# Kernel tuning notes

Measured on AMD Instinct MI355X. Metric: run time of the kernel, lower is better.

Reference implementation:

```python
import jax, jax.numpy as jnp
import numpy as np

B, S, D_IN, D_OUT = 4, 4096, 1024, 1024

def setup_inputs() -> dict:
    key = jax.random.key(0)
    kx, kq, kk, kv = jax.random.split(key, 4)
    x = jax.random.normal(kx, (B, S, D_IN), dtype=jnp.float32)
    # torch nn.Linear stores weight as [d_out, d_in]; y = x @ W.T
    Wq = jax.random.normal(kq, (D_OUT, D_IN), dtype=jnp.float32) * 0.02
    Wk = jax.random.normal(kk, (D_OUT, D_IN), dtype=jnp.float32) * 0.02
    Wv = jax.random.normal(kv, (D_OUT, D_IN), dtype=jnp.float32) * 0.02
    return {"x": x, "Wq": Wq, "Wk": Wk, "Wv": Wv}

def reference(x, Wq, Wk, Wv):
    b, n, _ = x.shape
    d_out = Wk.shape[0]
    q = jnp.einsum('bnd,od->bno', x, Wq)
    k = jnp.einsum('bnd,od->bno', x, Wk)
    v = jnp.einsum('bnd,od->bno', x, Wv)
    scores = jnp.einsum('bqo,bko->bqk', q, k)  # [B, S, S]
    causal = jnp.triu(jnp.ones((n, n), dtype=bool), k=1)
    scores = jnp.where(causal, -jnp.inf, scores)
    attn = jax.nn.softmax(scores / jnp.sqrt(jnp.float32(d_out)), axis=-1)
    # dropout p=0.0 -> identity
    return jnp.einsum('bqk,bko->bqo', attn, v)
```

## Files before the change

### kernel.cpp

```cpp
#include <hip/hip_runtime.h>


typedef unsigned short u16;
typedef unsigned int u32;
typedef __attribute__((ext_vector_type(8))) short bf16x8;
typedef __attribute__((ext_vector_type(4))) float f32x4;
typedef __attribute__((ext_vector_type(8))) unsigned short u16x8;

__device__ __forceinline__ u16 f2bf(float f) {
  union { float f; unsigned u; } v; v.f = f;
  unsigned r = v.u + 0x7FFFu + ((v.u >> 16) & 1u);
  return (u16)(r >> 16);
}
__device__ __forceinline__ float bf2f(u16 h) {
  union { unsigned u; float f; } v; v.u = ((unsigned)h) << 16;
  return v.f;
}
__device__ __forceinline__ f32x4 mfma16(bf16x8 a, bf16x8 b, f32x4 c) {
  return __builtin_amdgcn_mfma_f32_16x16x32_bf16(a, b, c, 0, 0, 0);
}
__device__ __forceinline__ void gld_lds16(const u16* g, u16* l) {
  __builtin_amdgcn_global_load_lds(
      (const __attribute__((address_space(1))) u32*)g,
      (__attribute__((address_space(3))) u32*)l, 16, 0, 0);
}
#define BAR() do { __builtin_amdgcn_s_barrier(); \
                   __builtin_amdgcn_sched_barrier(0); } while (0)
#define LGKM0() do { asm volatile("s_waitcnt lgkmcnt(0)" ::: "memory"); \
                     __builtin_amdgcn_sched_barrier(0); } while (0)
#define VMC(n) asm volatile("s_waitcnt vmcnt(" #n ")" ::: "memory")

__global__ __launch_bounds__(256)
void cast_all(const float* __restrict__ x, const float* __restrict__ Wq,
              const float* __restrict__ Wk, const float* __restrict__ Wv,
              u16* __restrict__ wX, u16* __restrict__ wWqkv) {
  int i = blockIdx.x * 256 + threadIdx.x;
  const float* src; u16* dst; int j;
  if (i < 2097152)        { src = x;  dst = wX;                j = i; }
  else if (i < 2228224)   { src = Wq; dst = wWqkv;             j = i - 2097152; }
  else if (i < 2359296)   { src = Wk; dst = wWqkv + 1048576;   j = i - 2228224; }
  else if (i < 2490368)   { src = Wv; dst = wWqkv + 2097152;   j = i - 2359296; }
  else return;
  const float4* s4 = (const float4*)src;
  float4 a = s4[2*j], b = s4[2*j+1];
  u16x8 o;
  o[0]=f2bf(a.x); o[1]=f2bf(a.y); o[2]=f2bf(a.z); o[3]=f2bf(a.w);
  o[4]=f2bf(b.x); o[5]=f2bf(b.y); o[6]=f2bf(b.z); o[7]=f2bf(b.w);
  ((u16x8*)dst)[j] = o;
}

#define GEMM8_CORE(Abase, Bbase)                                              \
  auto stageA = [&](int bufi, int h, int t) {                                 \
    _Pragma("unroll")                                                         \
    for (int i = 0; i < 2; ++i) {                                             \
      int ci = i * 512 + tid;                                                 \
      int r  = ci >> 3;                                                       \
      int c  = (ci & 7) ^ (r & 7);                                            \
      gld_lds16(Abase + (size_t)(h * 128 + r) * 1024 + t * 64 + c * 8,        \
                &At[bufi][h][ci * 8]);                                        \
    }                                                                         \
  };                                                                          \
  auto stageB = [&](int bufi, int h, int t) {                                 \
    _Pragma("unroll")                                                         \
    for (int i = 0; i < 2; ++i) {                                             \
      int ci = i * 512 + tid;                                                 \
      int r  = ci >> 3;                                                       \
      int c  = (ci & 7) ^ (r & 7);                                            \
      gld_lds16(Bbase + (size_t)(h * 128 + r) * 1024 + t * 64 + c * 8,        \
                &Bt[bufi][h][ci * 8]);                                        \
    }                                                                         \
  };                                                                          \
  bf16x8 af[8][2], bfr[4][2];                                                 \
  auto readA = [&](int bufi, int mb) {                                        \
    _Pragma("unroll")                                                         \
    for (int m = 0; m < 4; ++m)                                               \
      _Pragma("unroll")                                                       \
      for (int dk = 0; dk < 2; ++dk) {                                        \
        int r  = (mb + m) * 16 + c16;                                         \
        int ch = dk * 4 + g;                                                  \
        af[mb + m][dk] =                                                      \
            *(const bf16x8*)&At[bufi][wr][r * 64 + ((ch ^ (r & 7)) * 8)];     \
      }                                                                       \
  };                                                                          \
  auto readB = [&](int bufi, int nb) {                                        \
    _Pragma("unroll")                                                         \
    for (int n = 0; n < 2; ++n)                                               \
      _Pragma("unroll")                                                       \
      for (int dk = 0; dk < 2; ++dk) {                                        \
        int r  = (wc & 1) * 64 + (nb + n) * 16 + c16;                         \
        int ch = dk * 4 + g;                                                  \
        bfr[nb + n][dk] =                                                     \
            *(const bf16x8*)&Bt[bufi][wc >> 1][r * 64 + ((ch ^ (r & 7)) * 8)];\
      }                                                                       \
  };                                                                          \
  auto domfma = [&](int mb, int nb) {                                         \
    __builtin_amdgcn_s_setprio(1);                                            \
    _Pragma("unroll")                                                         \
    for (int dk = 0; dk < 2; ++dk)                                            \
      _Pragma("unroll")                                                       \
      for (int m = 0; m < 4; ++m)                                             \
        _Pragma("unroll")                                                     \
        for (int n = 0; n < 2; ++n)                                           \
          acc[mb + m][nb + n] =                                               \
              mfma16(af[mb + m][dk], bfr[nb + n][dk], acc[mb + m][nb + n]);   \
    __builtin_amdgcn_s_setprio(0);                                            \
  };                                                                          \
                   \
  stageA(0, 0, 0); stageA(0, 1, 0); stageB(0, 0, 0); stageB(0, 1, 0);         \
  stageA(1, 0, 1); stageA(1, 1, 1); stageB(1, 0, 1); stageB(1, 1, 1);         \
  VMC(8);                                         \
  BAR();                                                                      \
  for (int it = 0; it < 8; ++it) {                                            \
    const bool pf = (it < 7);                                                 \
    const int t2 = 2 * it + 2, t3 = 2 * it + 3;                               \
                                   \
    readA(0, 0); readB(0, 0);                                                 \
    BAR(); LGKM0();                                                           \
    domfma(0, 0);                                                             \
    BAR();                                                                    \
                                   \
    readA(0, 4);                                                              \
    BAR(); LGKM0();                                                           \
    domfma(4, 0);                                                             \
    BAR();                                                                    \
                     \
    readB(0, 2);                                                              \
    if (pf) { stageA(0, 0, t2); stageA(0, 1, t2); }                           \
    BAR(); LGKM0();                                                           \
    domfma(4, 2);                                                             \
    BAR();                                                                    \
                         \
    if (pf) { stageB(0, 0, t2); stageB(0, 1, t2); }                           \
    BAR();                                                                    \
    domfma(0, 2);                                                             \
    if (pf) { VMC(8); } else { VMC(0); }                                      \
    BAR();                                                                    \
                                                   \
    readA(1, 0); readB(1, 0);                                                 \
    BAR(); LGKM0();                                                           \
    domfma(0, 0);                                                             \
    BAR();                                                                    \
    readA(1, 4);                                                              \
    BAR(); LGKM0();                                                           \
    domfma(4, 0);                                                             \
    BAR();                                                                    \
    readB(1, 2);                                                              \
    if (pf) { stageA(1, 0, t3); stageA(1, 1, t3); }                           \
    BAR(); LGKM0();                                                           \
    domfma(4, 2);                                                             \
    BAR();                                                                    \
    if (pf) { stageB(1, 0, t3); stageB(1, 1, t3); }                           \
    BAR();                                                                    \
    domfma(0, 2);                                                             \
    if (pf) { VMC(8); } else { VMC(0); }                                      \
    BAR();                                                                    \
  }

__global__ __launch_bounds__(512, 1)
void qkv_gemm(const u16* __restrict__ X, const u16* __restrict__ W,
              u16* __restrict__ Qo, u16* __restrict__ Ko, u16* __restrict__ VTo) {
  __shared__ __align__(16) u16 At[2][2][128 * 64];
  __shared__ __align__(16) u16 Bt[2][2][128 * 64];
  const int tid = threadIdx.x;
  const int w = tid >> 6, lane = tid & 63;
  const int g = lane >> 4, c16 = lane & 15;
  const int wr = w >> 2, wc = w & 3;
  const int lid = blockIdx.x;
  const int xcd = lid & 7, gg = lid >> 3;
  const int M0 = ((xcd << 3) | (gg & 7)) * 256;
  const int N0 = (gg >> 3) * 256;
  const u16* Abase = X + (size_t)M0 * 1024;
  const u16* Bbase = W + (size_t)N0 * 1024;

  f32x4 acc[8][4] = {};
  GEMM8_CORE(Abase, Bbase);

  const int which = N0 >> 10;
  const int colbase = N0 & 1023;
#pragma unroll
  for (int m = 0; m < 8; ++m) {
#pragma unroll
    for (int n = 0; n < 4; ++n) {
#pragma unroll
      for (int r = 0; r < 4; ++r) {
        int gm  = M0 + wr * 128 + m * 16 + 4 * g + r;
        int col = colbase + wc * 64 + n * 16 + c16;
        u16 hv = f2bf(acc[m][n][r]);
        if (which == 0) {
          Qo[(size_t)gm * 1024 + col] = hv;
        } else if (which == 1) {
          Ko[(size_t)gm * 1024 + col] = hv;
        } else {
          int b = gm >> 12, s2 = gm & 4095;
          VTo[((size_t)((b << 10) + col)) * 4096 + s2] = hv;
        }
      }
    }
  }
}

__global__ __launch_bounds__(512, 1)
void sgemm_exp(const u16* __restrict__ Q, const u16* __restrict__ K,
               u16* __restrict__ Spack, float* __restrict__ lpart) {
  __shared__ __align__(16) u16 At[2][2][128 * 64];
  __shared__ __align__(16) u16 Bt[2][2][128 * 64];
  __shared__ float lsum[256][4];
  const int tid = threadIdx.x;
  const int w = tid >> 6, lane = tid & 63;
  const int g = lane >> 4, c16 = lane & 15;
  const int wr = w >> 2, wc = w & 3;
  const int b = blockIdx.y;

  int L = (blockIdx.x & 7) * 17 + (blockIdx.x >> 3);
  int qt = 0;
  while ((qt + 1) * (qt + 2) / 2 <= L) ++qt;
  const int kt = L - qt * (qt + 1) / 2;

  const u16* Abase = Q + (size_t)b * 4096 * 1024 + (size_t)qt * 256 * 1024;
  const u16* Bbase = K + (size_t)b * 4096 * 1024 + (size_t)kt * 256 * 1024;

  f32x4 acc[8][4] = {};
  GEMM8_CORE(Abase, Bbase);

  const int qt128 = 2 * qt + wr;
  const int kt128 = 2 * kt + (wc >> 1);
  const bool exists = (kt128 <= qt128);
  u16* Sb = Spack + (((size_t)b * 528 + (size_t)(qt128 * (qt128 + 1)) / 2 + kt128) << 14);
  const int q0 = qt * 256, k0g = kt * 256;
  float psum[8][4];
#pragma unroll
  for (int m = 0; m < 8; ++m)
#pragma unroll
    for (int r = 0; r < 4; ++r) psum[m][r] = 0.f;
#pragma unroll
  for (int m = 0; m < 8; ++m) {
#pragma unroll
    for (int n = 0; n < 4; ++n) {
#pragma unroll
      for (int r = 0; r < 4; ++r) {
        int rl = wr * 128 + m * 16 + 4 * g + r;
        int cl = wc * 64 + n * 16 + c16;
        float s = acc[m][n][r] * 0.03125f;
        float p = (k0g + cl <= q0 + rl) ? __expf(s) : 0.f;
        u16 pb = f2bf(p);
        if (exists) Sb[(rl & 127) * 128 + (cl & 127)] = pb;
        psum[m][r] += bf2f(pb);
      }
    }
  }
#pragma unroll
  for (int m = 0; m < 8; ++m)
#pragma unroll
    for (int r = 0; r < 4; ++r) {
      float v = psum[m][r];
      v += __shfl_xor(v, 1, 64);
      v += __shfl_xor(v, 2, 64);
      v += __shfl_xor(v, 4, 64);
      v += __shfl_xor(v, 8, 64);
      psum[m][r] = v;
    }
  if (c16 == 0) {
#pragma unroll
    for (int m = 0; m < 8; ++m)
#pragma unroll
      for (int r = 0; r < 4; ++r)
        lsum[wr * 128 + m * 16 + 4 * g + r][wc] = psum[m][r];
  }
  __syncthreads();
  if (tid < 256) {
    float v = lsum[tid][0] + lsum[tid][1] + lsum[tid][2] + lsum[tid][3];
    lpart[((size_t)b * 4096 + q0 + tid) * 16 + kt] = v;
  }
}

__global__ __launch_bounds__(512)
void pv_gemm(const u16* __restrict__ Spack, const u16* __restrict__ VT,
             const u16* __restrict__ ztile, const float* __restrict__ lpart,
             float* __restrict__ Out) {
  __shared__ __align__(16) u16 At[2][256 * 64];
  __shared__ __align__(16) u16 Bt[2][128 * 64];
  __shared__ float linv_lds[512];
  const int tid = threadIdx.x;
  const int w = tid >> 6, lane = tid & 63;
  const int g = lane >> 4, c16 = lane & 15;
  const int wm = w >> 1, wn = w & 1;
  const int pp = blockIdx.x;
  const int d0 = blockIdx.y;
  const int b  = blockIdx.z;

  const u16* Sp_b = Spack + (size_t)b * 528 * 16384;
  const u16* VTb  = VT + (size_t)b * 1024 * 4096;
  float* Ob = Out + (size_t)b * 4096 * 1024;

  {
    const int QTr = (tid < 256) ? pp : (15 - pp);
    const int row = QTr * 256 + (tid & 255);
    const int nt  = QTr + 1;
    const float* p = lpart + ((size_t)b * 4096 + row) * 16;
    float s = 0.f;
    for (int i = 0; i < nt; ++i) s += p[i];
    linv_lds[tid] = 1.f / s;
  }

  for (int pass = 0; pass < 2; ++pass) {
    const int QT = pass == 0 ? pp : 15 - pp;
    const int M0 = QT * 256;
    const int nsteps = (QT + 1) * 4;
    const int tLo = 2 * QT;
    const size_t triLo = (size_t)(tLo * (tLo + 1)) / 2;
    const size_t triHi = (size_t)((tLo + 1) * (tLo + 2)) / 2;

    f32x4 acc[4][4] = {};

    auto stage = [&](int s, int tt) {
      const int kv0 = tt * 64;
      const int kt128 = tt >> 1;
      const int koff = (tt & 1) * 64;
      const u16* baseLo = (kt128 <= tLo) ? Sp_b + ((triLo + kt128) << 14) : ztile;
      const u16* baseHi = Sp_b + ((triHi + kt128) << 14);
#pragma unroll
      for (int i = 0; i < 4; ++i) {
        int ci = i * 512 + tid;
        int r = ci >> 3;
        int c = (ci & 7) ^ (r & 7);
        const u16* base = (i < 2) ? baseLo : baseHi;
        gld_lds16(base + (size_t)(r & 127) * 128 + koff + c * 8, &At[s][ci * 8]);
      }
#pragma unroll
      for (int i = 0; i < 2; ++i) {
        int ci = i * 512 + tid;
        int r = ci >> 3;
        int c = (ci & 7) ^ (r & 7);
        gld_lds16(VTb + (size_t)(d0 * 128 + r) * 4096 + kv0 + c * 8, &Bt[s][ci * 8]);
      }
    };
    auto compute = [&](int s) {
#pragma unroll
      for (int dk = 0; dk < 2; ++dk) {
        bf16x8 af2[4], bf2[4];
#pragma unroll
        for (int m = 0; m < 4; ++m) {
          int row = wm * 64 + m * 16 + c16;
          int ch = dk * 4 + g;
          af2[m] = *(const bf16x8*)&At[s][row * 64 + ((ch ^ (row & 7)) * 8)];
        }
#pragma unroll
        for (int n = 0; n < 4; ++n) {
          int row = wn * 64 + n * 16 + c16;
          int ch = dk * 4 + g;
          bf2[n] = *(const bf16x8*)&Bt[s][row * 64 + ((ch ^ (row & 7)) * 8)];
        }
#pragma unroll
        for (int m = 0; m < 4; ++m)
#pragma unroll
          for (int n = 0; n < 4; ++n)
            acc[m][n] = mfma16(af2[m], bf2[n], acc[m][n]);
      }
    };

    stage(0, 0);
    __syncthreads();
    int cur = 0;
    for (int t = 0; t < nsteps; ++t) {
      if (t + 1 < nsteps) stage(cur ^ 1, t + 1);
      compute(cur);
      __syncthreads();
      cur ^= 1;
    }

    const float* lb = linv_lds + pass * 256;
#pragma unroll
    for (int m = 0; m < 4; ++m) {
#pragma unroll
      for (int r = 0; r < 4; ++r) {
        int rl = wm * 64 + m * 16 + 4 * g + r;
        float li = lb[rl];
#pragma unroll
        for (int n = 0; n < 4; ++n) {
          int dcol = d0 * 128 + wn * 64 + n * 16 + c16;
          Ob[(size_t)(M0 + rl) * 1024 + dcol] = acc[m][n][r] * li;
        }
      }
    }
  }
}

__global__ __launch_bounds__(512, 2)
void attn_kernel(const u16* __restrict__ Q, const u16* __restrict__ K,
                 const u16* __restrict__ VT, float* __restrict__ Out) {
  __shared__ u16 kv_lds[32 * 1024];
  __shared__ float s_part[4][32][33];
  __shared__ u16 p_lds[32 * 40];
  __shared__ float l_lds[32];

  const int tid = threadIdx.x;
  const int w = tid >> 6, lane = tid & 63;
  const int g = lane >> 4, c16 = lane & 15;
  const int b  = blockIdx.x & 3;
  const int qb = 127 - (blockIdx.x >> 2);
  const int qs = qb * 32;
  const int kh = w & 1, dq = w >> 1;

  const u16* Qb  = Q  + (size_t)b * 4096 * 1024;
  const u16* Kb  = K  + (size_t)b * 4096 * 1024;
  const u16* VTb = VT + (size_t)b * 1024 * 4096;

  bf16x8 qfrag[2][8];
#pragma unroll
  for (int qh = 0; qh < 2; ++qh)
#pragma unroll
    for (int dk = 0; dk < 8; ++dk)
      qfrag[qh][dk] = *(const bf16x8*)(Qb + (size_t)(qs + qh * 16 + c16) * 1024
                                       + dq * 256 + dk * 32 + g * 8);

  f32x4 oacc[2][8] = {};
  if (tid < 32) l_lds[tid] = 0.f;

  const int qrow_p = tid >> 4;
  const int kk     = tid & 15;
  const int gq     = qs + qrow_p;

  for (int j = 0; j <= qb; ++j) {
    const int kv0 = j * 32;
    __syncthreads();
    uint4 rk[8];
#pragma unroll
    for (int i = 0; i < 8; ++i) {
      int ci = i * 512 + tid;
      int r  = ci >> 7;
      int c  = (ci & 127) ^ (r & 7);
      rk[i] = *(const uint4*)(Kb + (size_t)(kv0 + r) * 1024 + c * 8);
    }
#pragma unroll
    for (int i = 0; i < 8; ++i)
      *(uint4*)&kv_lds[(size_t)(i * 512 + tid) * 8] = rk[i];
    __syncthreads();
    f32x4 sacc[2] = {};
#pragma unroll
    for (int dk = 0; dk < 8; ++dk) {
      int kvrow = kh * 16 + c16;
      int ch    = dq * 32 + dk * 4 + g;
      bf16x8 kf = *(const bf16x8*)&kv_lds[kvrow * 1024 + ((ch ^ (kvrow & 7)) * 8)];
      sacc[0] = mfma16(qfrag[0][dk], kf, sacc[0]);
      sacc[1] = mfma16(qfrag[1][dk], kf, sacc[1]);
    }
#pragma unroll
    for (int qh = 0; qh < 2; ++qh)
#pragma unroll
      for (int r = 0; r < 4; ++r)
        s_part[dq][qh * 16 + 4 * g + r][kh * 16 + c16] = sacc[qh][r];
    __syncthreads();
    uint4 rv[8];
#pragma unroll
    for (int i = 0; i < 8; ++i) {
      int ci = i * 512 + tid;
      int d  = ((ci >> 6) << 4) + (ci & 15);
      int c  = (ci >> 4) & 3;
      rv[i] = *(const uint4*)(VTb + (size_t)d * 4096 + kv0 + c * 8);
    }
    {
      float psum = 0.f;
#pragma unroll
      for (int h = 0; h < 2; ++h) {
        int kcol = kk + h * 16;
        float s = s_part[0][qrow_p][kcol] + s_part[1][qrow_p][kcol]
                + s_part[2][qrow_p][kcol] + s_part[3][qrow_p][kcol];
        s *= 0.03125f;
        float p = (kv0 + kcol <= gq) ? __expf(s) : 0.f;
        u16 pb = f2bf(p);
        p_lds[qrow_p * 40 + kcol] = pb;
        psum += bf2f(pb);
      }
#pragma unroll
      for (int off = 1; off < 16; off <<= 1)
        psum += __shfl_xor(psum, off, 64);
      if (kk == 0) l_lds[qrow_p] += psum;
    }
#pragma unroll
    for (int i = 0; i < 8; ++i)
      *(uint4*)&kv_lds[(size_t)(i * 512 + tid) * 8] = rv[i];
    __syncthreads();
    bf16x8 pa0 = *(const bf16x8*)&p_lds[(0  + c16) * 40 + g * 8];
    bf16x8 pa1 = *(const bf16x8*)&p_lds[(16 + c16) * 40 + g * 8];
#pragma unroll
    for (int f = 0; f < 8; ++f) {
      int dcol = w * 128 + f * 16 + c16;
      int pos  = (dcol >> 4) * 64 + g * 16 + (dcol & 15);
      bf16x8 vf = *(const bf16x8*)&kv_lds[(size_t)pos * 8];
      oacc[0][f] = mfma16(pa0, vf, oacc[0][f]);
      oacc[1][f] = mfma16(pa1, vf, oacc[1][f]);
    }
  }

  float* Ob = Out + (size_t)b * 4096 * 1024;
#pragma unroll
  for (int qh = 0; qh < 2; ++qh) {
#pragma unroll
    for (int r = 0; r < 4; ++r) {
      int ql = qh * 16 + 4 * g + r;
      float linvv = 1.f / l_lds[ql];
#pragma unroll
      for (int f = 0; f < 8; ++f)
        Ob[(size_t)(qs + ql) * 1024 + w * 128 + f * 16 + c16] = oacc[qh][f][r] * linvv;
    }
  }
}

extern "C" void kernel_launch(void* const* d_in, const int* in_sizes, int n_in,
                              void* d_out, int out_size, void* d_ws, size_t ws_size,
                              hipStream_t stream) {
  const float* x  = (const float*)d_in[0];
  const float* Wq = (const float*)d_in[1];
  const float* Wk = (const float*)d_in[2];
  const float* Wv = (const float*)d_in[3];
  float* out = (float*)d_out;

  u16* ws    = (u16*)d_ws;
  u16* wWqkv = ws;
  u16* wX    = wWqkv + (size_t)3 * 1024 * 1024;
  u16* wQ    = wX + (size_t)16384 * 1024;
  u16* wK    = wQ + (size_t)16384 * 1024;
  u16* wVT   = wK + (size_t)16384 * 1024;
  u16* wSp   = wVT + (size_t)16384 * 1024;
  float* lpart = (float*)(ws + (size_t)104857600);

  cast_all<<<dim3(9728), 256, 0, stream>>>(x, Wq, Wk, Wv, wX, wWqkv);

  qkv_gemm<<<dim3(768), 512, 0, stream>>>(wX, wWqkv, wQ, wK, wVT);

  if (ws_size >= (size_t)211877888) {
    hipMemsetAsync(wX, 0, 32768, stream);
    sgemm_exp<<<dim3(136, 4), 512, 0, stream>>>(wQ, wK, wSp, lpart);
    pv_gemm<<<dim3(8, 8, 4), 512, 0, stream>>>(wSp, wVT, wX, lpart, out);
  } else {
    attn_kernel<<<dim3(512), 512, 0, stream>>>(wQ, wK, wVT, out);
  }
}
```

Baseline: 368.0 us.

## Restructure pv_gemm main loop into quadrant-interleaved ping-pong schedule

Replaces pv_gemm's simple double-buffered stage/compute loop with the same fine-grained schedule used by the QK kernel. It splits LDS reads and MFMAs into 2x2 sub-tile quadrants, interleaves global-to-LDS prefetch of the next tile between them, and uses explicit barriers, vmcnt waits and setprio. It also sets launch_bounds to one block per CU. The goal is to hide global load latency behind MFMA work and keep the matrix units busy. In exchange it adds many more barriers per step and may raise register pressure.

After: 356.1 us. 3.2% less time.

```diff
diff --git a/kernel.cpp b/kernel.cpp
--- a/kernel.cpp
+++ b/kernel.cpp
@@ -105,37 +105,31 @@
               mfma16(af[mb + m][dk], bfr[nb + n][dk], acc[mb + m][nb + n]);   \
     __builtin_amdgcn_s_setprio(0);                                            \
   };                                                                          \
-                   \
   stageA(0, 0, 0); stageA(0, 1, 0); stageB(0, 0, 0); stageB(0, 1, 0);         \
   stageA(1, 0, 1); stageA(1, 1, 1); stageB(1, 0, 1); stageB(1, 1, 1);         \
-  VMC(8);                                         \
+  VMC(8);                                                                     \
   BAR();                                                                      \
   for (int it = 0; it < 8; ++it) {                                            \
     const bool pf = (it < 7);                                                 \
     const int t2 = 2 * it + 2, t3 = 2 * it + 3;                               \
-                                   \
     readA(0, 0); readB(0, 0);                                                 \
     BAR(); LGKM0();                                                           \
     domfma(0, 0);                                                             \
     BAR();                                                                    \
-                                   \
     readA(0, 4);                                                              \
     BAR(); LGKM0();                                                           \
     domfma(4, 0);                                                             \
     BAR();                                                                    \
-                     \
     readB(0, 2);                                                              \
     if (pf) { stageA(0, 0, t2); stageA(0, 1, t2); }                           \
     BAR(); LGKM0();                                                           \
     domfma(4, 2);                                                             \
     BAR();                                                                    \
-                         \
     if (pf) { stageB(0, 0, t2); stageB(0, 1, t2); }                           \
     BAR();                                                                    \
     domfma(0, 2);                                                             \
     if (pf) { VMC(8); } else { VMC(0); }                                      \
     BAR();                                                                    \
-                                                   \
     readA(1, 0); readB(1, 0);                                                 \
     BAR(); LGKM0();                                                           \
     domfma(0, 0);                                                             \
@@ -273,7 +267,7 @@
   }
 }
 
-__global__ __launch_bounds__(512)
+__global__ __launch_bounds__(512, 1)
 void pv_gemm(const u16* __restrict__ Spack, const u16* __restrict__ VT,
              const u16* __restrict__ ztile, const float* __restrict__ lpart,
              float* __restrict__ Out) {
@@ -306,66 +300,114 @@
     const int QT = pass == 0 ? pp : 15 - pp;
     const int M0 = QT * 256;
     const int nsteps = (QT + 1) * 4;
+    const int niter  = nsteps >> 1;
     const int tLo = 2 * QT;
     const size_t triLo = (size_t)(tLo * (tLo + 1)) / 2;
     const size_t triHi = (size_t)((tLo + 1) * (tLo + 2)) / 2;
 
     f32x4 acc[4][4] = {};
 
-    auto stage = [&](int s, int tt) {
-      const int kv0 = tt * 64;
+    auto stA = [&](int bufi, int half, int tt) {
       const int kt128 = tt >> 1;
       const int koff = (tt & 1) * 64;
-      const u16* baseLo = (kt128 <= tLo) ? Sp_b + ((triLo + kt128) << 14) : ztile;
-      const u16* baseHi = Sp_b + ((triHi + kt128) << 14);
-#pragma unroll
-      for (int i = 0; i < 4; ++i) {
-        int ci = i * 512 + tid;
+      const u16* base;
+      if (half == 0) base = (kt128 <= tLo) ? Sp_b + ((triLo + kt128) << 14) : ztile;
+      else           base = Sp_b + ((triHi + kt128) << 14);
+#pragma unroll
+      for (int i = 0; i < 2; ++i) {
+        int ci = (half * 2 + i) * 512 + tid;
         int r = ci >> 3;
         int c = (ci & 7) ^ (r & 7);
-        const u16* base = (i < 2) ? baseLo : baseHi;
-        gld_lds16(base + (size_t)(r & 127) * 128 + koff + c * 8, &At[s][ci * 8]);
+        gld_lds16(base + (size_t)(r & 127) * 128 + koff + c * 8, &At[bufi][ci * 8]);
       }
+    };
+    auto stB = [&](int bufi, int tt) {
+      const int kv0 = tt * 64;
 #pragma unroll
       for (int i = 0; i < 2; ++i) {
         int ci = i * 512 + tid;
         int r = ci >> 3;
         int c = (ci & 7) ^ (r & 7);
-        gld_lds16(VTb + (size_t)(d0 * 128 + r) * 4096 + kv0 + c * 8, &Bt[s][ci * 8]);
+        gld_lds16(VTb + (size_t)(d0 * 128 + r) * 4096 + kv0 + c * 8, &Bt[bufi][ci * 8]);
       }
     };
-    auto compute = [&](int s) {
-#pragma unroll
-      for (int dk = 0; dk < 2; ++dk) {
-        bf16x8 af2[4], bf2[4];
-#pragma unroll
-        for (int m = 0; m < 4; ++m) {
-          int row = wm * 64 + m * 16 + c16;
+
+    bf16x8 af[4][2], bfr[4][2];
+    auto readA = [&](int bufi, int mb) {
+#pragma unroll
+      for (int m = 0; m < 2; ++m)
+#pragma unroll
+        for (int dk = 0; dk < 2; ++dk) {
+          int row = wm * 64 + (mb + m) * 16 + c16;
           int ch = dk * 4 + g;
-          af2[m] = *(const bf16x8*)&At[s][row * 64 + ((ch ^ (row & 7)) * 8)];
+          af[mb + m][dk] = *(const bf16x8*)&At[bufi][row * 64 + ((ch ^ (row & 7)) * 8)];
         }
-#pragma unroll
-        for (int n = 0; n < 4; ++n) {
-          int row = wn * 64 + n * 16 + c16;
+    };
+    auto readB = [&](int bufi, int nb) {
+#pragma unroll
+      for (int n = 0; n < 2; ++n)
+#pragma unroll
+        for (int dk = 0; dk < 2; ++dk) {
+          int row = wn * 64 + (nb + n) * 16 + c16;
           int ch = dk * 4 + g;
-          bf2[n] = *(const bf16x8*)&Bt[s][row * 64 + ((ch ^ (row & 7)) * 8)];
+          bfr[nb + n][dk] = *(const bf16x8*)&Bt[bufi][row * 64 + ((ch ^ (row & 7)) * 8)];
         }
-#pragma unroll
-        for (int m = 0; m < 4; ++m)
-#pragma unroll
-          for (int n = 0; n < 4; ++n)
-            acc[m][n] = mfma16(af2[m], bf2[n], acc[m][n]);
-      }
     };
-
-    stage(0, 0);
-    __syncthreads();
-    int cur = 0;
-    for (int t = 0; t < nsteps; ++t) {
-      if (t + 1 < nsteps) stage(cur ^ 1, t + 1);
-      compute(cur);
-      __syncthreads();
-      cur ^= 1;
+    auto domfma = [&](int mb, int nb) {
+      __builtin_amdgcn_s_setprio(1);
+#pragma unroll
+      for (int dk = 0; dk < 2; ++dk)
+#pragma unroll
+        for (int m = 0; m < 2; ++m)
+#pragma unroll
+          for (int n = 0; n < 2; ++n)
+            acc[mb + m][nb + n] = mfma16(af[mb + m][dk], bfr[nb + n][dk], acc[mb + m][nb + n]);
+      __builtin_amdgcn_s_setprio(0);
+    };
+
+    stA(0, 0, 0); stA(0, 1, 0); stB(0, 0);
+    stA(1, 0, 1); stA(1, 1, 1); stB(1, 1);
+    VMC(6);
+    BAR();
+    for (int it = 0; it < niter; ++it) {
+      const bool pf = (it + 1 < niter);
+      const int t2 = 2 * it + 2, t3 = 2 * it + 3;
+      readA(0, 0); readB(0, 0);
+      BAR(); LGKM0();
+      domfma(0, 0);
+      BAR();
+      readA(0, 2);
+      BAR(); LGKM0();
+      domfma(2, 0);
+      BAR();
+      readB(0, 2);
+      if (pf) { stA(0, 0, t2); stA(0, 1, t2); }
+      BAR(); LGKM0();
+      domfma(2, 2);
+      BAR();
+      if (pf) stB(0, t2);
+      BAR();
+      domfma(0, 2);
+      if (pf) { VMC(6); } else { VMC(0); }
+      BAR();
+      readA(1, 0); readB(1, 0);
+      BAR(); LGKM0();
+      domfma(0, 0);
+      BAR();
+      readA(1, 2);
+      BAR(); LGKM0();
+      domfma(2, 0);
+      BAR();
+      readB(1, 2);
+      if (pf) { stA(1, 0, t3); stA(1, 1, t3); }
+      BAR(); LGKM0();
+      domfma(2, 2);
+      BAR();
+      if (pf) stB(1, t3);
+      BAR();
+      domfma(0, 2);
+      if (pf) { VMC(6); } else { VMC(0); }
+      BAR();
     }
 
     const float* lb = linv_lds + pass * 256;
```
